# Optimization experiments

Measured on AMD Instinct MI355X. Metric: run time of the kernel, lower is better.

The kernel has to match this reference:

```python
import jax, jax.numpy as jnp
import numpy as np

B, S, I, H, O = 64, 1024, 256, 512, 256


def setup_inputs() -> dict:
    key = jax.random.key(0)
    ks = jax.random.split(key, 13)
    s = 0.02
    return {
        "x": jax.random.normal(ks[0], (B, S, I), dtype=jnp.float32),
        "U_w": jax.random.normal(ks[1], (H, I), dtype=jnp.float32) * s,
        "U_b": jax.random.normal(ks[2], (H,), dtype=jnp.float32) * s,
        "W_w": jax.random.normal(ks[3], (H, H), dtype=jnp.float32) * s,
        "W_b": jax.random.normal(ks[4], (H,), dtype=jnp.float32) * s,
        "V_w": jax.random.normal(ks[5], (H, H), dtype=jnp.float32) * s,
        "V_b": jax.random.normal(ks[6], (H,), dtype=jnp.float32) * s,
        "fc1_w": jax.random.normal(ks[7], (H, H), dtype=jnp.float32) * s,
        "fc1_b": jax.random.normal(ks[8], (H,), dtype=jnp.float32) * s,
        "fc2_w": jax.random.normal(ks[9], (H, H), dtype=jnp.float32) * s,
        "fc2_b": jax.random.normal(ks[10], (H,), dtype=jnp.float32) * s,
        "fc3_w": jax.random.normal(ks[11], (O, H), dtype=jnp.float32) * s,
        "fc3_b": jax.random.normal(ks[12], (O,), dtype=jnp.float32) * s,
    }


def reference(x, U_w, U_b, W_w, W_b, V_w, V_b, fc1_w, fc1_b, fc2_w, fc2_b, fc3_w, fc3_b):
    # x: [B, S, I] (batch_first). Time-major for the recurrence: [S, B, I]
    xt = jnp.swapaxes(x, 0, 1)
    # Input projection U(x_t) is time-independent: precompute once. [S, B, H]
    xu = jnp.einsum('sbi,hi->sbh', xt, U_w) + U_b

    def step(h_prev, xu_t):
        # a_t = U x_t + W h_{t-1}; h_t = tanh(a_t); o_t = V h_t
        h_t = jnp.tanh(xu_t + h_prev @ W_w.T + W_b)
        o_t = h_t @ V_w.T + V_b
        return h_t, o_t

    h0 = jnp.zeros((x.shape[0], W_w.shape[0]), dtype=x.dtype)
    _, out = jax.lax.scan(step, h0, xu)  # out: [S, B, H]

    # MLP head (dropout layers are identity in eval mode)
    out = out @ fc1_w.T + fc1_b
    out = out @ fc2_w.T + fc2_b
    out = out @ fc3_w.T + fc3_b  # [S, B, O]
    return jnp.swapaxes(out, 0, 1)  # [B, S, O]
```

## Files before the change

kernel.cpp:

```cpp
#include <hip/hip_runtime.h>
#include <hip/hip_bf16.h>

typedef __attribute__((ext_vector_type(8))) short short8;
typedef __attribute__((ext_vector_type(4))) float f32x4;

#define B_ 64
#define S_ 1024
#define I_ 256
#define H_ 512
#define O_ 256
#define M_ (B_ * S_)
#define SC 2.8853900817779268f

__device__ __forceinline__ ushort bf16_rne(float f) {
  unsigned u = __float_as_uint(f);
  return (ushort)((u + 0x7FFFu + ((u >> 16) & 1u)) >> 16);
}
__device__ __forceinline__ float bf16_f(ushort s) {
  return __uint_as_float(((unsigned)s) << 16);
}
__device__ __forceinline__ unsigned cvt_pk_bf16(float lo, float hi) {
  unsigned r;
  asm("v_cvt_pk_bf16_f32 %0, %1, %2" : "=v"(r) : "v"(lo), "v"(hi));
  return r;
}
__device__ __forceinline__ void gll16(const void* g, void* l) {
  __builtin_amdgcn_global_load_lds((const __attribute__((address_space(1))) void*)g,
                                   (__attribute__((address_space(3))) void*)l, 16, 0, 0);
}
__device__ __forceinline__ float tanh_pre(float a) {
#if __has_builtin(__builtin_amdgcn_exp2f)
  float t = __builtin_amdgcn_exp2f(fminf(a, 26.0f));
#else
  float t = exp2f(fminf(a, 26.0f));
#endif
#if __has_builtin(__builtin_amdgcn_rcpf)
  return (t - 1.0f) * __builtin_amdgcn_rcpf(t + 1.0f);
#else
  return (t - 1.0f) / (t + 1.0f);
#endif
}

__global__ void cvt_kern(const float* __restrict__ in, ushort* __restrict__ out, long n,
                         float scale) {
  long i = ((long)blockIdx.x * blockDim.x + threadIdx.x) * 4;
  const long stride = (long)gridDim.x * blockDim.x * 4;
  for (; i < n; i += stride) {
    const float4 v = *(const float4*)(in + i);
    ushort4 o;
    o.x = bf16_rne(v.x * scale); o.y = bf16_rne(v.y * scale);
    o.z = bf16_rne(v.z * scale); o.w = bf16_rne(v.w * scale);
    *(ushort4*)(out + i) = o;
  }
}

__global__ void biascomb_kern(const float* __restrict__ a, const float* __restrict__ b,
                              float* __restrict__ o) {
  int i = threadIdx.x;
  o[i] = (a[i] + b[i]) * SC;
}

__global__ __launch_bounds__(256) void f32gemm_kern(
    const float* __restrict__ A, const float* __restrict__ Bm,
    float* __restrict__ C, int M, int N, int K)
{
  __shared__ float As[16][16];
  __shared__ float Bs[16][17];
  const int tx = threadIdx.x & 15, ty = threadIdx.x >> 4;
  const int row = blockIdx.y * 16 + ty, col = blockIdx.x * 16 + tx;
  float acc = 0.0f;
  for (int k0 = 0; k0 < K; k0 += 16) {
    As[ty][tx] = A[(size_t)row * K + k0 + tx];
    Bs[ty][tx] = Bm[(size_t)(k0 + ty) * N + col];
    __syncthreads();
    #pragma unroll
    for (int kk = 0; kk < 16; ++kk) acc += As[ty][kk] * Bs[kk][tx];
    __syncthreads();
  }
  C[(size_t)row * N + col] = acc;
}

__global__ void matvec_kern(const float* __restrict__ Mw, const float* __restrict__ x,
                            const float* __restrict__ b, float* __restrict__ y, int R, int C) {
  const int wid = (int)((blockIdx.x * blockDim.x + threadIdx.x) >> 6);
  const int lane = threadIdx.x & 63;
  if (wid >= R) return;
  float acc = 0.0f;
  for (int k = lane; k < C; k += 64) acc += Mw[(size_t)wid * C + k] * x[k];
  #pragma unroll
  for (int off = 32; off; off >>= 1) acc += __shfl_down(acc, off, 64);
  if (lane == 0) y[wid] = acc + b[wid];
}

template<bool OUT_F32>
__global__ __launch_bounds__(256) void gemm_kern(
    const ushort* __restrict__ A, const ushort* __restrict__ Wt,
    const float* __restrict__ bias, void* __restrict__ out,
    int M, int N, int K)
{
  __shared__ char smem[16384];
  const int tid = threadIdx.x;
  const int lane = tid & 63, wave = tid >> 6;
  const int wm = wave >> 1, wn = wave & 1;
  const int nt = N >> 7;
  const int bm = blockIdx.x / nt, bn = blockIdx.x % nt;
  const long m0 = (long)bm * 128, n0 = (long)bn * 128;

  f32x4 acc[4][4] = {};
  const int KT = K >> 5;
  for (int kt = 0; kt < KT; ++kt) {
    #pragma unroll
    for (int i = 0; i < 4; ++i) {
      const int c = wave * 4 + i;
      const int isB = c >> 3;
      const int cc = c & 7;
      const int kgrp = cc >> 1, rhalf = cc & 1;
      const int row = rhalf * 64 + lane;
      const ushort* src = (isB ? Wt + (n0 + row) * (long)K : A + (m0 + row) * (long)K)
                          + (long)kt * 32 + kgrp * 8;
      gll16(src, smem + isB * 8192 + kgrp * 2048 + rhalf * 1024);
    }
    __syncthreads();
    const char* Ab = smem + (lane >> 4) * 2048;
    const char* Bb = smem + 8192 + (lane >> 4) * 2048;
    short8 af[4], bf[4];
    #pragma unroll
    for (int i = 0; i < 4; ++i) {
      af[i] = *(const short8*)(Ab + (wm * 64 + i * 16 + (lane & 15)) * 16);
      bf[i] = *(const short8*)(Bb + (wn * 64 + i * 16 + (lane & 15)) * 16);
    }
    #pragma unroll
    for (int mi = 0; mi < 4; ++mi)
      #pragma unroll
      for (int ni = 0; ni < 4; ++ni)
        acc[mi][ni] = __builtin_amdgcn_mfma_f32_16x16x32_bf16(af[mi], bf[ni], acc[mi][ni], 0, 0, 0);
    __syncthreads();
  }
  #pragma unroll
  for (int ni = 0; ni < 4; ++ni) {
    const long n = n0 + wn * 64 + ni * 16 + (lane & 15);
    const float bv = bias[n];
    #pragma unroll
    for (int mi = 0; mi < 4; ++mi) {
      const long mrow = m0 + wm * 64 + mi * 16 + (lane >> 4) * 4;
      #pragma unroll
      for (int r = 0; r < 4; ++r) {
        const float v = acc[mi][ni][r] + bv;
        if (OUT_F32) ((float*)out)[(mrow + r) * (long)N + n] = v;
        else         ((ushort*)out)[(mrow + r) * (long)N + n] = bf16_rne(v);
      }
    }
  }
}

__global__ __launch_bounds__(512, 2) void rec_kern(
    const ushort* __restrict__ XU,
    const ushort* __restrict__ Wb,
    ushort* __restrict__ Hst)
{
  extern __shared__ char smem[];
  const int tid = threadIdx.x;
  const int lane = tid & 63;
  const int wave = tid >> 6;
  const int b = lane & 15;
  const int hi = lane >> 4;
  const int bg = blockIdx.x << 4;
  const int swz = (b & 7) << 4;

  #pragma unroll
  for (int i = 0; i < 16; ++i) {
    const int ch = wave * 16 + i;
    const int s = 12 + (ch >> 5);
    const int mt = ch & 31;
    const ushort* src = Wb + (size_t)(mt * 16 + b) * H_ + s * 32 + hi * 8;
    gll16(src, smem + 32768 + (size_t)(s - 12) * 32768 + mt * 1024);
  }
  {
    f32x4 zz = 0.0f;
    *(f32x4*)(smem + tid * 64) = zz;
    *(f32x4*)(smem + tid * 64 + 16) = zz;
    *(f32x4*)(smem + tid * 64 + 32) = zz;
    *(f32x4*)(smem + tid * 64 + 48) = zz;
  }
  short8 wreg[4][12];
  #pragma unroll
  for (int mt = 0; mt < 4; ++mt) {
    const int mtg = wave * 4 + mt;
    const ushort* wrow = Wb + (size_t)(mtg * 16 + b) * H_ + hi * 8;
    #pragma unroll
    for (int s = 0; s < 12; ++s)
      wreg[mt][s] = *(const short8*)(wrow + s * 32);
  }
  #pragma unroll
  for (int mt = 0; mt < 4; ++mt)
    #pragma unroll
    for (int s = 0; s < 12; ++s)
      asm volatile("" : "+v"(wreg[mt][s]));
  __syncthreads();

  const ushort* xup = XU + (size_t)(bg + b) * S_ * H_ + wave * 64 + hi * 4;
  ushort* hgp = Hst + (size_t)(bg + b) * S_ * H_ + wave * 64 + hi * 4;
  const int hoff = b * 1024;
  const int woff = (wave * 128 + hi * 8);

  for (int t = 0; t < S_; ++t) {
    uint2 xu[4];
    #pragma unroll
    for (int mt = 0; mt < 4; ++mt)
      xu[mt] = *(const uint2*)(xup + mt * 16);
    xup += H_;

    const char* hb = smem + (t & 1) * 16384 + hoff;
    f32x4 acc[4] = {};
    #pragma unroll
    for (int s = 0; s < 16; ++s) {
      const short8 bfrag = *(const short8*)(hb + ((s * 64 + hi * 16) ^ swz));
      #pragma unroll
      for (int mt = 0; mt < 4; ++mt) {
        short8 w;
        if (s < 12) w = wreg[mt][s];
        else w = *(const short8*)(smem + 32768 + (s - 12) * 32768 + (wave * 4 + mt) * 1024 + lane * 16);
        acc[mt] = __builtin_amdgcn_mfma_f32_16x16x32_bf16(w, bfrag, acc[mt], 0, 0, 0);
      }
    }
    char* hw = smem + ((t + 1) & 1) * 16384 + hoff;
    #pragma unroll
    for (int mt = 0; mt < 4; ++mt) {
      const float h0 = tanh_pre(acc[mt][0] + bf16_f((ushort)(xu[mt].x & 0xFFFFu)));
      const float h1 = tanh_pre(acc[mt][1] + bf16_f((ushort)(xu[mt].x >> 16)));
      const float h2 = tanh_pre(acc[mt][2] + bf16_f((ushort)(xu[mt].y & 0xFFFFu)));
      const float h3 = tanh_pre(acc[mt][3] + bf16_f((ushort)(xu[mt].y >> 16)));
      uint2 hv;
      hv.x = cvt_pk_bf16(h0, h1);
      hv.y = cvt_pk_bf16(h2, h3);
      *(uint2*)(hw + ((woff + mt * 32) ^ swz)) = hv;
      *(uint2*)(hgp + mt * 16) = hv;
    }
    hgp += H_;
    __syncthreads();
  }
}

extern "C" void kernel_launch(void* const* d_in, const int* in_sizes, int n_in,
                              void* d_out, int out_size, void* d_ws, size_t ws_size,
                              hipStream_t stream) {
  const float* x     = (const float*)d_in[0];
  const float* U_w   = (const float*)d_in[1];
  const float* U_b   = (const float*)d_in[2];
  const float* W_w   = (const float*)d_in[3];
  const float* W_b   = (const float*)d_in[4];
  const float* V_w   = (const float*)d_in[5];
  const float* V_b   = (const float*)d_in[6];
  const float* fc1_w = (const float*)d_in[7];
  const float* fc1_b = (const float*)d_in[8];
  const float* fc2_w = (const float*)d_in[9];
  const float* fc2_b = (const float*)d_in[10];
  const float* fc3_w = (const float*)d_in[11];
  const float* fc3_b = (const float*)d_in[12];

  char* ws = (char*)d_ws;
  ushort* Hst  = (ushort*)ws;
  ushort* xb16 = (ushort*)(ws + 67108864);
  char*   wb   = ws + 134217728;
  ushort* U_wb = (ushort*)wb;
  ushort* W_wb = U_wb + 131072;
  ushort* Wcb  = W_wb + 262144;
  float*  C1   = (float*)(Wcb + 131072);
  float*  C2   = C1 + 262144;
  float*  Wcf  = C2 + 262144;
  float*  cbias = Wcf + 131072;
  float*  t1   = cbias + 512;
  float*  t2   = t1 + 512;
  float*  bc   = t2 + 512;
  ushort* bufA = (ushort*)d_out;

  cvt_kern<<<2048, 256, 0, stream>>>(x, xb16, (long)M_ * I_, 1.0f);
  cvt_kern<<<128, 256, 0, stream>>>(U_w, U_wb, (long)H_ * I_, SC);
  cvt_kern<<<256, 256, 0, stream>>>(W_w, W_wb, (long)H_ * H_, SC);
  biascomb_kern<<<1, 512, 0, stream>>>(U_b, W_b, cbias);

  f32gemm_kern<<<dim3(32, 32), 256, 0, stream>>>(fc1_w, V_w, C1, H_, H_, H_);
  f32gemm_kern<<<dim3(32, 32), 256, 0, stream>>>(fc2_w, C1, C2, H_, H_, H_);
  f32gemm_kern<<<dim3(32, 16), 256, 0, stream>>>(fc3_w, C2, Wcf, O_, H_, H_);
  matvec_kern<<<128, 256, 0, stream>>>(fc1_w, V_b, fc1_b, t1, H_, H_);
  matvec_kern<<<128, 256, 0, stream>>>(fc2_w, t1, fc2_b, t2, H_, H_);
  matvec_kern<<<64, 256, 0, stream>>>(fc3_w, t2, fc3_b, bc, O_, H_);
  cvt_kern<<<128, 256, 0, stream>>>(Wcf, Wcb, (long)O_ * H_, 1.0f);

  gemm_kern<false><<<dim3(512 * 4), 256, 0, stream>>>(xb16, U_wb, cbias, bufA, M_, H_, I_);

  hipFuncSetAttribute((const void*)rec_kern, hipFuncAttributeMaxDynamicSharedMemorySize, 163840);
  rec_kern<<<dim3(4), dim3(512), 163840, stream>>>(bufA, W_wb, Hst);

  gemm_kern<true><<<dim3(512 * 2), 256, 0, stream>>>(Hst, Wcb, bc, d_out, M_, O_, H_);

  (void)in_sizes; (void)n_in; (void)out_size; (void)ws_size;
}
```

Before: 2.503 ms.

## Stream unpinned recurrent weight slices from global/L2 instead of LDS

The recurrent kernel now keeps 9 of 16 K-slices of W in registers instead of 12. The remaining slices are no longer staged in LDS; they are loaded from global memory (expected to hit in cache) each timestep with a two-slice prefetch and scheduling barriers. This frees register pressure and shrinks dynamic LDS from 160KB to 32KB. The cost is global loads on the sequential critical path every step, which add latency to a strictly serial loop.

```diff
diff --git a/kernel.cpp b/kernel.cpp
--- a/kernel.cpp
+++ b/kernel.cpp
@@ -11,6 +11,7 @@
 #define O_ 256
 #define M_ (B_ * S_)
 #define SC 2.8853900817779268f
+#define NPIN 9
 
 __device__ __forceinline__ ushort bf16_rne(float f) {
   unsigned u = __float_as_uint(f);
@@ -167,14 +168,6 @@
   const int bg = blockIdx.x << 4;
   const int swz = (b & 7) << 4;
 
-  #pragma unroll
-  for (int i = 0; i < 16; ++i) {
-    const int ch = wave * 16 + i;
-    const int s = 12 + (ch >> 5);
-    const int mt = ch & 31;
-    const ushort* src = Wb + (size_t)(mt * 16 + b) * H_ + s * 32 + hi * 8;
-    gll16(src, smem + 32768 + (size_t)(s - 12) * 32768 + mt * 1024);
-  }
   {
     f32x4 zz = 0.0f;
     *(f32x4*)(smem + tid * 64) = zz;
@@ -182,20 +175,24 @@
     *(f32x4*)(smem + tid * 64 + 32) = zz;
     *(f32x4*)(smem + tid * 64 + 48) = zz;
   }
-  short8 wreg[4][12];
+  short8 wreg[4][NPIN];
   #pragma unroll
   for (int mt = 0; mt < 4; ++mt) {
     const int mtg = wave * 4 + mt;
     const ushort* wrow = Wb + (size_t)(mtg * 16 + b) * H_ + hi * 8;
     #pragma unroll
-    for (int s = 0; s < 12; ++s)
+    for (int s = 0; s < NPIN; ++s)
       wreg[mt][s] = *(const short8*)(wrow + s * 32);
   }
   #pragma unroll
   for (int mt = 0; mt < 4; ++mt)
     #pragma unroll
-    for (int s = 0; s < 12; ++s)
+    for (int s = 0; s < NPIN; ++s)
       asm volatile("" : "+v"(wreg[mt][s]));
+  const ushort* wmt[4];
+  #pragma unroll
+  for (int mt = 0; mt < 4; ++mt)
+    wmt[mt] = Wb + (size_t)((wave * 4 + mt) * 16 + b) * H_ + hi * 8;
   __syncthreads();
 
   const ushort* xup = XU + (size_t)(bg + b) * S_ * H_ + wave * 64 + hi * 4;
@@ -210,16 +207,26 @@
       xu[mt] = *(const uint2*)(xup + mt * 16);
     xup += H_;
 
+    short8 ws[16 - NPIN][4];
+    #pragma unroll
+    for (int mt = 0; mt < 4; ++mt) ws[0][mt] = *(const short8*)(wmt[mt] + NPIN * 32);
+    #pragma unroll
+    for (int mt = 0; mt < 4; ++mt) ws[1][mt] = *(const short8*)(wmt[mt] + (NPIN + 1) * 32);
+
     const char* hb = smem + (t & 1) * 16384 + hoff;
     f32x4 acc[4] = {};
     #pragma unroll
     for (int s = 0; s < 16; ++s) {
+      if (s >= NPIN && s + 2 < 16) {
+        __builtin_amdgcn_sched_barrier(0x38F);
+        #pragma unroll
+        for (int mt = 0; mt < 4; ++mt)
+          ws[s + 2 - NPIN][mt] = *(const short8*)(wmt[mt] + (s + 2) * 32);
+      }
       const short8 bfrag = *(const short8*)(hb + ((s * 64 + hi * 16) ^ swz));
       #pragma unroll
       for (int mt = 0; mt < 4; ++mt) {
-        short8 w;
-        if (s < 12) w = wreg[mt][s];
-        else w = *(const short8*)(smem + 32768 + (s - 12) * 32768 + (wave * 4 + mt) * 1024 + lane * 16);
+        const short8 w = (s < NPIN) ? wreg[mt][s] : ws[s - NPIN][mt];
         acc[mt] = __builtin_amdgcn_mfma_f32_16x16x32_bf16(w, bfrag, acc[mt], 0, 0, 0);
       }
     }
@@ -289,8 +296,8 @@
 
   gemm_kern<false><<<dim3(512 * 4), 256, 0, stream>>>(xb16, U_wb, cbias, bufA, M_, H_, I_);
 
-  hipFuncSetAttribute((const void*)rec_kern, hipFuncAttributeMaxDynamicSharedMemorySize, 163840);
-  rec_kern<<<dim3(4), dim3(512), 163840, stream>>>(bufA, W_wb, Hst);
+  hipFuncSetAttribute((const void*)rec_kern, hipFuncAttributeMaxDynamicSharedMemorySize, 32768);
+  rec_kern<<<dim3(4), dim3(512), 32768, stream>>>(bufA, W_wb, Hst);
 
   gemm_kern<true><<<dim3(512 * 2), 256, 0, stream>>>(Hst, Wcb, bc, d_out, M_, O_, H_);
 
```

Measured after the change: 5.813 ms. +132.2%, slower.
